# Kernel optimization log

Measured on AMD Instinct MI355X. Metric: run time of the kernel, lower is better.

## Reference

```python
import jax, jax.numpy as jnp
import numpy as np

NUM_HEADS = 16
BLOCK_KV = 64


def _split_heads(x, h):
    B, T, D = x.shape
    return x.reshape(B, T, h, D // h).transpose(0, 2, 1, 3)  # [B,H,T,Hd]


def _merge_heads(x):
    B, H, T, Hd = x.shape
    return x.transpose(0, 2, 1, 3).reshape(B, T, H * Hd)


def _streaming_attention(qh, kh, vh, bkv):
    # Online-softmax (flash-attention) over kv blocks; math identical to the
    # original nested-loop version (including the Z + 1e-9 denominator).
    B, H, T, Dh = qh.shape
    scale = 1.0 / jnp.sqrt(Dh).astype(jnp.float32)
    q32 = qh.astype(jnp.float32)
    nb = T // bkv
    # [nb, B, H, bkv, Dh]
    kb = jnp.moveaxis(kh.astype(jnp.float32).reshape(B, H, nb, bkv, Dh), 2, 0)
    vb = jnp.moveaxis(vh.astype(jnp.float32).reshape(B, H, nb, bkv, Dh), 2, 0)

    def step(carry, blk):
        m, Z, O = carry
        k_blk, v_blk = blk
        scores = jnp.einsum('bhtd,bhkd->bhtk', q32, k_blk) * scale
        m_new = jnp.maximum(m, jnp.max(scores, axis=-1, keepdims=True))
        alpha = jnp.exp(m - m_new)
        p = jnp.exp(scores - m_new)
        Z = Z * alpha + jnp.sum(p, axis=-1, keepdims=True)
        O = O * alpha + jnp.einsum('bhtk,bhkd->bhtd', p, v_blk)
        return (m_new, Z, O), None

    m0 = jnp.full((B, H, T, 1), -jnp.inf, dtype=jnp.float32)
    Z0 = jnp.zeros((B, H, T, 1), dtype=jnp.float32)
    O0 = jnp.zeros((B, H, T, Dh), dtype=jnp.float32)
    (m, Z, O), _ = jax.lax.scan(step, (m0, Z0, O0), (kb, vb))
    return (O / (Z + 1e-9)).astype(qh.dtype)


def setup_inputs() -> dict:
    key = jax.random.key(0)
    ks = jax.random.split(key, 6)
    B, T, D = 4, 8192, 512
    s = 1.0 / np.sqrt(D)
    return {
        'x': jax.random.normal(ks[0], (B, T, D), dtype=jnp.float32),
        'Wq': jax.random.normal(ks[1], (D, D), dtype=jnp.float32) * s,
        'Wk': jax.random.normal(ks[2], (D, D), dtype=jnp.float32) * s,
        'Wv': jax.random.normal(ks[3], (D, D), dtype=jnp.float32) * s,
        'Wo': jax.random.normal(ks[4], (D, D), dtype=jnp.float32) * s,
        'bo': jnp.zeros((D,), dtype=jnp.float32),
    }


def reference(x, Wq, Wk, Wv, Wo, bo):
    q = x @ Wq
    k = x @ Wk
    v = x @ Wv
    qh = _split_heads(q, NUM_HEADS)
    kh = _split_heads(k, NUM_HEADS)
    vh = _split_heads(v, NUM_HEADS)
    out_h = _streaming_attention(qh, kh, vh, BLOCK_KV)
    return _merge_heads(out_h) @ Wo + bo
```

## Files before the change

kernel.cpp:

```cpp
#include <hip/hip_runtime.h>
#include <hip/hip_bf16.h>
#include <math.h>

typedef __bf16 bf16;
typedef __bf16 bf16x2 __attribute__((ext_vector_type(2)));
typedef __bf16 bf16x4 __attribute__((ext_vector_type(4)));
typedef __bf16 bf16x8 __attribute__((ext_vector_type(8)));
typedef float f32x4 __attribute__((ext_vector_type(4)));
typedef unsigned int u32;
typedef u32 u32x4 __attribute__((ext_vector_type(4)));

#define B_ 4
#define T_ 8192
#define D_ 512
#define H_ 16
#define HD_ 32
#define M_ (B_ * T_)

#if __has_builtin(__builtin_amdgcn_exp2f)
#define EXP2(x) __builtin_amdgcn_exp2f(x)
#else
#define EXP2(x) exp2f(x)
#endif

#define LDSP(p) ((__attribute__((address_space(3))) void*)(p))
#define GLBP(p) ((const __attribute__((address_space(1))) void*)(p))

static __device__ __forceinline__ u32 pkbf16(float a, float b) {
  bf16x2 t;
  t[0] = (bf16)a;
  t[1] = (bf16)b;
  return __builtin_bit_cast(u32, t);
}

static __device__ __forceinline__ void swap32(u32& a, u32& b) {
#if __has_builtin(__builtin_amdgcn_permlane32_swap)
  auto r = __builtin_amdgcn_permlane32_swap(a, b, false, false);
  a = r[0];
  b = r[1];
#else
  asm volatile("v_permlane32_swap_b32 %0, %1" : "+v"(a), "+v"(b));
#endif
}

__global__ void k_cvt(const float* __restrict__ in, bf16* __restrict__ out, int n4) {
  int i = blockIdx.x * blockDim.x + threadIdx.x;
  const int stride = gridDim.x * blockDim.x;
  for (; i < n4; i += stride) {
    const float4 v = ((const float4*)in)[i];
    bf16x4 o;
    o.x = (bf16)v.x; o.y = (bf16)v.y; o.z = (bf16)v.z; o.w = (bf16)v.w;
    ((bf16x4*)out)[i] = o;
  }
}

__global__ void k_cvt_T(const float* __restrict__ w, bf16* __restrict__ wT, float scale) {
  const int tid = blockIdx.x * blockDim.x + threadIdx.x;
  const int n = tid >> 9, k = tid & 511;
  wT[tid] = (bf16)(w[k * 512 + n] * scale);
}

__global__ __launch_bounds__(256) void k_transposeV(const bf16* __restrict__ V,
                                                    bf16* __restrict__ VT) {
  __shared__ bf16 tile[128][36];
  const int bh = blockIdx.y, chunk = blockIdx.x;
  const int b = bh >> 4, h = bh & 15;
  const int kv0 = chunk * 128;
  const int tid = threadIdx.x;
  const int r = tid >> 1, c0 = (tid & 1) * 16;
  const size_t ib = ((size_t)(b * T_ + kv0 + r)) * 512 + h * 32 + c0;
  *(bf16x8*)&tile[r][c0]     = *(const bf16x8*)&V[ib];
  *(bf16x8*)&tile[r][c0 + 8] = *(const bf16x8*)&V[ib + 8];
  __syncthreads();
  const int d = tid >> 3, j0 = (tid & 7) * 16;
  bf16x8 o0, o1;
#pragma unroll
  for (int i = 0; i < 4; ++i) {
    o0[i]     = tile[j0 + i][d];
    o0[i + 4] = tile[j0 + 8 + i][d];
    o1[i]     = tile[j0 + 4 + i][d];
    o1[i + 4] = tile[j0 + 12 + i][d];
  }
  const size_t ob = ((size_t)bh * 32 + d) * T_ + kv0 + j0;
  *(bf16x8*)&VT[ob] = o0;
  *(bf16x8*)&VT[ob + 8] = o1;
}

template <int OUTF32>
__global__ __launch_bounds__(256) void k_gemm(const bf16* __restrict__ A,
                                              const bf16* __restrict__ BT,
                                              void* __restrict__ Cout,
                                              const float* __restrict__ bias) {
  __shared__ bf16 As[128][40];
  __shared__ bf16 Bs[128][40];
  const int bn = blockIdx.x * 128;
  const int bm = blockIdx.y * 128;
  const int tid = threadIdx.x;
  const int l = tid & 63, wid = tid >> 6;
  const int ln = l & 15, ku = l >> 4;
  const int wm = (wid >> 1) * 64, wn = (wid & 1) * 64;
  const int sr = tid >> 2, sc = (tid & 3) * 8;

  f32x4 acc[4][4] = {};

  for (int ks = 0; ks < 512; ks += 32) {
    __syncthreads();
    *(bf16x8*)&As[sr][sc]      = *(const bf16x8*)&A[(size_t)(bm + sr) * 512 + ks + sc];
    *(bf16x8*)&As[sr + 64][sc] = *(const bf16x8*)&A[(size_t)(bm + sr + 64) * 512 + ks + sc];
    *(bf16x8*)&Bs[sr][sc]      = *(const bf16x8*)&BT[(size_t)(bn + sr) * 512 + ks + sc];
    *(bf16x8*)&Bs[sr + 64][sc] = *(const bf16x8*)&BT[(size_t)(bn + sr + 64) * 512 + ks + sc];
    __syncthreads();

    bf16x8 af[4], bfr[4];
#pragma unroll
    for (int mt = 0; mt < 4; ++mt) af[mt] = *(const bf16x8*)&As[wm + mt * 16 + ln][ku * 8];
#pragma unroll
    for (int nt = 0; nt < 4; ++nt) bfr[nt] = *(const bf16x8*)&Bs[wn + nt * 16 + ln][ku * 8];
#pragma unroll
    for (int mt = 0; mt < 4; ++mt)
#pragma unroll
      for (int nt = 0; nt < 4; ++nt)
        acc[mt][nt] = __builtin_amdgcn_mfma_f32_16x16x32_bf16(af[mt], bfr[nt], acc[mt][nt], 0, 0, 0);
  }

#pragma unroll
  for (int mt = 0; mt < 4; ++mt)
#pragma unroll
    for (int nt = 0; nt < 4; ++nt)
#pragma unroll
      for (int r = 0; r < 4; ++r) {
        const int row = bm + wm + mt * 16 + ku * 4 + r;
        const int col = bn + wn + nt * 16 + ln;
        const float v = acc[mt][nt][r];
        if (OUTF32)
          ((float*)Cout)[(size_t)row * 512 + col] = v + bias[col];
        else
          ((bf16*)Cout)[(size_t)row * 512 + col] = (bf16)v;
      }
}

__global__ __launch_bounds__(256, 5) void k_attn(const bf16* __restrict__ Q,
                                                 const bf16* __restrict__ K,
                                                 const bf16* __restrict__ VT,
                                                 bf16* __restrict__ O) {
  __shared__ bf16 ks[2][2][64][32];
  __shared__ bf16 vts[2][2][32][64];
  const int qt = blockIdx.x;
  const int bh = blockIdx.y;
  const int b = bh >> 4, h = bh & 15;
  const size_t base = (size_t)b * T_ * 512 + (size_t)h * 32;
  const size_t vtbase = (size_t)bh * 32 * T_;
  const int tid = threadIdx.x;
  const int l = tid & 63, w = tid >> 6;
  const int ln = l & 15, ku = l >> 4;

  const int q0 = qt * 128 + w * 32;
  bf16x8 qf[2];
#pragma unroll
  for (int j = 0; j < 2; ++j)
    qf[j] = *(const bf16x8*)&Q[base + (size_t)(q0 + j * 16 + ln) * 512 + ku * 8];

  const u32 one2 = 0x3F803F80u;
  u32x4 onesu = {one2, one2, one2, one2};
  const bf16x8 ones = __builtin_bit_cast(bf16x8, onesu);

  const int krow = tid >> 2;
  const int kchS = ((tid & 3) ^ ((krow >> 1) & 3)) * 8;
  const int vrow = tid >> 3;
  const int vchS = ((tid & 7) ^ (vrow & 7)) * 8;
  const bf16* gk = K + base + (size_t)krow * 512 + kchS;
  const bf16* gv = VT + vtbase + (size_t)vrow * T_ + vchS;

  bf16* dk0 = &ks[0][0][w * 16][0];
  bf16* dk1 = &ks[1][0][w * 16][0];
  bf16* dv0 = &vts[0][0][w * 8][0];
  bf16* dv1 = &vts[1][0][w * 8][0];

  const char* ksr = (const char*)&ks[0][0][0][0] + ln * 64 + 16 * (ku ^ ((ln >> 1) & 3));
  const char* vr0 = (const char*)&vts[0][0][0][0] + ln * 128 + 16 * ((ku) ^ (ln & 7));
  const char* vr1 = (const char*)&vts[0][0][0][0] + ln * 128 + 16 * ((4 + ku) ^ (ln & 7));

  f32x4 o[2][2] = {};
  f32x4 zacc[2] = {};

  __builtin_amdgcn_global_load_lds(GLBP(gk), LDSP(dk0), 16, 0, 0);
  __builtin_amdgcn_global_load_lds(GLBP(gk + 32768), LDSP(dk0 + 2048), 16, 0, 0);
  __builtin_amdgcn_global_load_lds(GLBP(gv), LDSP(dv0), 16, 0, 0);
  __builtin_amdgcn_global_load_lds(GLBP(gv + 64), LDSP(dv0 + 2048), 16, 0, 0);
  gk += 2 * 64 * 512;
  gv += 128;
  __syncthreads();

#define KV_BODY2(CUR, DKN, DVN)                                                         \
  {                                                                                     \
    __builtin_amdgcn_global_load_lds(GLBP(gk), LDSP(DKN), 16, 0, 0);                    \
    __builtin_amdgcn_global_load_lds(GLBP(gk + 32768), LDSP(DKN + 2048), 16, 0, 0);     \
    __builtin_amdgcn_global_load_lds(GLBP(gv), LDSP(DVN), 16, 0, 0);                    \
    __builtin_amdgcn_global_load_lds(GLBP(gv + 64), LDSP(DVN + 2048), 16, 0, 0);        \
    gk += 2 * 64 * 512;                                                                 \
    gv += 128;                                                                          \
    _Pragma("unroll") for (int sub = 0; sub < 2; ++sub) {                               \
      _Pragma("unroll") for (int j = 0; j < 2; ++j) {                                   \
        _Pragma("unroll") for (int c = 0; c < 2; ++c) {                                 \
          const bf16x8 kf0 =                                                            \
              *(const bf16x8*)(ksr + (CUR)*8192 + sub * 4096 + c * 2048);               \
          const bf16x8 kf1 =                                                            \
              *(const bf16x8*)(ksr + (CUR)*8192 + sub * 4096 + c * 2048 + 1024);        \
          const f32x4 zz = {};                                                          \
          f32x4 s0 = __builtin_amdgcn_mfma_f32_16x16x32_bf16(kf0, qf[j], zz, 0, 0, 0);  \
          f32x4 s1 = __builtin_amdgcn_mfma_f32_16x16x32_bf16(kf1, qf[j], zz, 0, 0, 0);  \
          u32 lo0 = pkbf16(EXP2(s0[0]), EXP2(s0[1]));                                   \
          u32 hi0 = pkbf16(EXP2(s0[2]), EXP2(s0[3]));                                   \
          u32 lo1 = pkbf16(EXP2(s1[0]), EXP2(s1[1]));                                   \
          u32 hi1 = pkbf16(EXP2(s1[2]), EXP2(s1[3]));                                   \
          swap32(lo0, lo1);                                                             \
          swap32(hi0, hi1);                                                             \
          u32x4 pd = {lo0, hi0, lo1, hi1};                                              \
          const bf16x8 pf = __builtin_bit_cast(bf16x8, pd);                             \
          const bf16x8 va0 =                                                            \
              *(const bf16x8*)((c ? vr1 : vr0) + (CUR)*8192 + sub * 4096);              \
          const bf16x8 va1 =                                                            \
              *(const bf16x8*)((c ? vr1 : vr0) + (CUR)*8192 + sub * 4096 + 2048);       \
          o[j][0] = __builtin_amdgcn_mfma_f32_16x16x32_bf16(va0, pf, o[j][0], 0, 0, 0); \
          o[j][1] = __builtin_amdgcn_mfma_f32_16x16x32_bf16(va1, pf, o[j][1], 0, 0, 0); \
          zacc[j] =                                                                     \
              __builtin_amdgcn_mfma_f32_16x16x32_bf16(ones, pf, zacc[j], 0, 0, 0);      \
        }                                                                               \
      }                                                                                 \
    }                                                                                   \
    __syncthreads();                                                                    \
  }

  for (int kb = 0; kb < 128; kb += 4) {
    KV_BODY2(0, dk1, dv1);
    KV_BODY2(1, dk0, dv0);
  }
#undef KV_BODY2

#pragma unroll
  for (int j = 0; j < 2; ++j) {
    const float iz = 1.0f / (zacc[j][0] + 1e-9f);
    bf16x4 w0, w1;
#pragma unroll
    for (int r = 0; r < 4; ++r) {
      w0[r] = (bf16)(o[j][0][r] * iz);
      w1[r] = (bf16)(o[j][1][r] * iz);
    }
    const size_t row = base + (size_t)(q0 + j * 16 + ln) * 512;
    *(bf16x4*)&O[row + ku * 4] = w0;
    *(bf16x4*)&O[row + 16 + ku * 4] = w1;
  }
}

extern "C" void kernel_launch(void* const* d_in, const int* in_sizes, int n_in,
                              void* d_out, int out_size, void* d_ws, size_t ws_size,
                              hipStream_t stream) {
  const float* x = (const float*)d_in[0];
  const float* Wq = (const float*)d_in[1];
  const float* Wk = (const float*)d_in[2];
  const float* Wv = (const float*)d_in[3];
  const float* Wo = (const float*)d_in[4];
  const float* bo = (const float*)d_in[5];
  float* out = (float*)d_out;

  char* ws = (char*)d_ws;
  const size_t SZ = (size_t)M_ * 512 * sizeof(bf16);
  bf16* xb = (bf16*)(ws);
  bf16* qb = (bf16*)(ws + SZ);
  bf16* kb = (bf16*)(ws + 2 * SZ);
  bf16* vb = (bf16*)(ws + 3 * SZ);
  bf16* ob = (bf16*)(ws + 4 * SZ);
  bf16* wqT = (bf16*)(ws + 5 * SZ);
  bf16* wkT = wqT + 512 * 512;
  bf16* wvT = wkT + 512 * 512;
  bf16* woT = wvT + 512 * 512;
  bf16* vt = xb;

  const float SCALE_L2E = 0.17677669529663687f * 1.4426950408889634f;

  k_cvt<<<2048, 256, 0, stream>>>(x, xb, M_ * 512 / 4);
  k_cvt_T<<<1024, 256, 0, stream>>>(Wq, wqT, SCALE_L2E);
  k_cvt_T<<<1024, 256, 0, stream>>>(Wk, wkT, 1.0f);
  k_cvt_T<<<1024, 256, 0, stream>>>(Wv, wvT, 1.0f);
  k_cvt_T<<<1024, 256, 0, stream>>>(Wo, woT, 1.0f);

  dim3 gg(4, 256);
  k_gemm<0><<<gg, 256, 0, stream>>>(xb, wqT, qb, nullptr);
  k_gemm<0><<<gg, 256, 0, stream>>>(xb, wkT, kb, nullptr);
  k_gemm<0><<<gg, 256, 0, stream>>>(xb, wvT, vb, nullptr);

  dim3 gt(64, 64);
  k_transposeV<<<gt, 256, 0, stream>>>(vb, vt);
  dim3 ga(64, 64);
  k_attn<<<ga, 256, 0, stream>>>(qb, kb, vt, ob);

  k_gemm<1><<<gg, 256, 0, stream>>>(ob, woT, out, bo);
}
```

Baseline: 821.5 us.

## Fuse Q/K/V projections into one GEMM and prioritize MFMA waves in attention

```diff
diff --git a/kernel.cpp b/kernel.cpp
--- a/kernel.cpp
+++ b/kernel.cpp
@@ -16,6 +16,7 @@
 #define H_ 16
 #define HD_ 32
 #define M_ (B_ * T_)
+#define QKVS 1536
 
 #if __has_builtin(__builtin_amdgcn_exp2f)
 #define EXP2(x) __builtin_amdgcn_exp2f(x)
@@ -54,13 +55,23 @@
   }
 }
 
+__global__ void k_cvt_T3(const float* __restrict__ Wq, const float* __restrict__ Wk,
+                         const float* __restrict__ Wv, bf16* __restrict__ wT,
+                         float scaleq) {
+  const int tid = blockIdx.x * blockDim.x + threadIdx.x;
+  const int n = tid >> 9, k = tid & 511;
+  const float* W = (n < 512) ? Wq : ((n < 1024) ? Wk : Wv);
+  const float sc = (n < 512) ? scaleq : 1.0f;
+  wT[tid] = (bf16)(W[k * 512 + (n & 511)] * sc);
+}
+
 __global__ void k_cvt_T(const float* __restrict__ w, bf16* __restrict__ wT, float scale) {
   const int tid = blockIdx.x * blockDim.x + threadIdx.x;
   const int n = tid >> 9, k = tid & 511;
   wT[tid] = (bf16)(w[k * 512 + n] * scale);
 }
 
-__global__ __launch_bounds__(256) void k_transposeV(const bf16* __restrict__ V,
+__global__ __launch_bounds__(256) void k_transposeV(const bf16* __restrict__ QKV,
                                                     bf16* __restrict__ VT) {
   __shared__ bf16 tile[128][36];
   const int bh = blockIdx.y, chunk = blockIdx.x;
@@ -68,9 +79,9 @@
   const int kv0 = chunk * 128;
   const int tid = threadIdx.x;
   const int r = tid >> 1, c0 = (tid & 1) * 16;
-  const size_t ib = ((size_t)(b * T_ + kv0 + r)) * 512 + h * 32 + c0;
-  *(bf16x8*)&tile[r][c0]     = *(const bf16x8*)&V[ib];
-  *(bf16x8*)&tile[r][c0 + 8] = *(const bf16x8*)&V[ib + 8];
+  const size_t ib = (size_t)(b * T_ + kv0 + r) * QKVS + 1024 + h * 32 + c0;
+  *(bf16x8*)&tile[r][c0]     = *(const bf16x8*)&QKV[ib];
+  *(bf16x8*)&tile[r][c0 + 8] = *(const bf16x8*)&QKV[ib + 8];
   __syncthreads();
   const int d = tid >> 3, j0 = (tid & 7) * 16;
   bf16x8 o0, o1;
@@ -90,7 +101,8 @@
 __global__ __launch_bounds__(256) void k_gemm(const bf16* __restrict__ A,
                                               const bf16* __restrict__ BT,
                                               void* __restrict__ Cout,
-                                              const float* __restrict__ bias) {
+                                              const float* __restrict__ bias,
+                                              int cstride) {
   __shared__ bf16 As[128][40];
   __shared__ bf16 Bs[128][40];
   const int bn = blockIdx.x * 128;
@@ -133,14 +145,13 @@
         const int col = bn + wn + nt * 16 + ln;
         const float v = acc[mt][nt][r];
         if (OUTF32)
-          ((float*)Cout)[(size_t)row * 512 + col] = v + bias[col];
+          ((float*)Cout)[(size_t)row * cstride + col] = v + bias[col];
         else
-          ((bf16*)Cout)[(size_t)row * 512 + col] = (bf16)v;
+          ((bf16*)Cout)[(size_t)row * cstride + col] = (bf16)v;
       }
 }
 
-__global__ __launch_bounds__(256, 5) void k_attn(const bf16* __restrict__ Q,
-                                                 const bf16* __restrict__ K,
+__global__ __launch_bounds__(256, 5) void k_attn(const bf16* __restrict__ QKV,
                                                  const bf16* __restrict__ VT,
                                                  bf16* __restrict__ O) {
   __shared__ bf16 ks[2][2][64][32];
@@ -148,7 +159,8 @@
   const int qt = blockIdx.x;
   const int bh = blockIdx.y;
   const int b = bh >> 4, h = bh & 15;
-  const size_t base = (size_t)b * T_ * 512 + (size_t)h * 32;
+  const size_t baseq = (size_t)b * T_ * QKVS + h * 32;
+  const size_t baseo = (size_t)b * T_ * 512 + h * 32;
   const size_t vtbase = (size_t)bh * 32 * T_;
   const int tid = threadIdx.x;
   const int l = tid & 63, w = tid >> 6;
@@ -158,7 +170,7 @@
   bf16x8 qf[2];
 #pragma unroll
   for (int j = 0; j < 2; ++j)
-    qf[j] = *(const bf16x8*)&Q[base + (size_t)(q0 + j * 16 + ln) * 512 + ku * 8];
+    qf[j] = *(const bf16x8*)&QKV[baseq + (size_t)(q0 + j * 16 + ln) * QKVS + ku * 8];
 
   const u32 one2 = 0x3F803F80u;
   u32x4 onesu = {one2, one2, one2, one2};
@@ -168,8 +180,9 @@
   const int kchS = ((tid & 3) ^ ((krow >> 1) & 3)) * 8;
   const int vrow = tid >> 3;
   const int vchS = ((tid & 7) ^ (vrow & 7)) * 8;
-  const bf16* gk = K + base + (size_t)krow * 512 + kchS;
+  const bf16* gk = QKV + baseq + 512 + (size_t)krow * QKVS + kchS;
   const bf16* gv = VT + vtbase + (size_t)vrow * T_ + vchS;
+  const int KSUB = 64 * QKVS;
 
   bf16* dk0 = &ks[0][0][w * 16][0];
   bf16* dk1 = &ks[1][0][w * 16][0];
@@ -184,20 +197,20 @@
   f32x4 zacc[2] = {};
 
   __builtin_amdgcn_global_load_lds(GLBP(gk), LDSP(dk0), 16, 0, 0);
-  __builtin_amdgcn_global_load_lds(GLBP(gk + 32768), LDSP(dk0 + 2048), 16, 0, 0);
+  __builtin_amdgcn_global_load_lds(GLBP(gk + KSUB), LDSP(dk0 + 2048), 16, 0, 0);
   __builtin_amdgcn_global_load_lds(GLBP(gv), LDSP(dv0), 16, 0, 0);
   __builtin_amdgcn_global_load_lds(GLBP(gv + 64), LDSP(dv0 + 2048), 16, 0, 0);
-  gk += 2 * 64 * 512;
+  gk += 2 * KSUB;
   gv += 128;
   __syncthreads();
 
 #define KV_BODY2(CUR, DKN, DVN)                                                         \
   {                                                                                     \
     __builtin_amdgcn_global_load_lds(GLBP(gk), LDSP(DKN), 16, 0, 0);                    \
-    __builtin_amdgcn_global_load_lds(GLBP(gk + 32768), LDSP(DKN + 2048), 16, 0, 0);     \
+    __builtin_amdgcn_global_load_lds(GLBP(gk + KSUB), LDSP(DKN + 2048), 16, 0, 0);      \
     __builtin_amdgcn_global_load_lds(GLBP(gv), LDSP(DVN), 16, 0, 0);                    \
     __builtin_amdgcn_global_load_lds(GLBP(gv + 64), LDSP(DVN + 2048), 16, 0, 0);        \
-    gk += 2 * 64 * 512;                                                                 \
+    gk += 2 * KSUB;                                                                     \
     gv += 128;                                                                          \
     _Pragma("unroll") for (int sub = 0; sub < 2; ++sub) {                               \
       _Pragma("unroll") for (int j = 0; j < 2; ++j) {                                   \
@@ -207,8 +220,10 @@
           const bf16x8 kf1 =                                                            \
               *(const bf16x8*)(ksr + (CUR)*8192 + sub * 4096 + c * 2048 + 1024);        \
           const f32x4 zz = {};                                                          \
+          __builtin_amdgcn_s_setprio(1);                                                \
           f32x4 s0 = __builtin_amdgcn_mfma_f32_16x16x32_bf16(kf0, qf[j], zz, 0, 0, 0);  \
           f32x4 s1 = __builtin_amdgcn_mfma_f32_16x16x32_bf16(kf1, qf[j], zz, 0, 0, 0);  \
+          __builtin_amdgcn_s_setprio(0);                                                \
           u32 lo0 = pkbf16(EXP2(s0[0]), EXP2(s0[1]));                                   \
           u32 hi0 = pkbf16(EXP2(s0[2]), EXP2(s0[3]));                                   \
           u32 lo1 = pkbf16(EXP2(s1[0]), EXP2(s1[1]));                                   \
@@ -221,10 +236,12 @@
               *(const bf16x8*)((c ? vr1 : vr0) + (CUR)*8192 + sub * 4096);              \
           const bf16x8 va1 =                                                            \
               *(const bf16x8*)((c ? vr1 : vr0) + (CUR)*8192 + sub * 4096 + 2048);       \
+          __builtin_amdgcn_s_setprio(1);                                                \
           o[j][0] = __builtin_amdgcn_mfma_f32_16x16x32_bf16(va0, pf, o[j][0], 0, 0, 0); \
           o[j][1] = __builtin_amdgcn_mfma_f32_16x16x32_bf16(va1, pf, o[j][1], 0, 0, 0); \
           zacc[j] =                                                                     \
               __builtin_amdgcn_mfma_f32_16x16x32_bf16(ones, pf, zacc[j], 0, 0, 0);      \
+          __builtin_amdgcn_s_setprio(0);                                                \
         }                                                                               \
       }                                                                                 \
     }                                                                                   \
@@ -246,7 +263,7 @@
       w0[r] = (bf16)(o[j][0][r] * iz);
       w1[r] = (bf16)(o[j][1][r] * iz);
     }
-    const size_t row = base + (size_t)(q0 + j * 16 + ln) * 512;
+    const size_t row = baseo + (size_t)(q0 + j * 16 + ln) * 512;
     *(bf16x4*)&O[row + ku * 4] = w0;
     *(bf16x4*)&O[row + 16 + ku * 4] = w1;
   }
@@ -266,33 +283,26 @@
   char* ws = (char*)d_ws;
   const size_t SZ = (size_t)M_ * 512 * sizeof(bf16);
   bf16* xb = (bf16*)(ws);
-  bf16* qb = (bf16*)(ws + SZ);
-  bf16* kb = (bf16*)(ws + 2 * SZ);
-  bf16* vb = (bf16*)(ws + 3 * SZ);
+  bf16* qkv = (bf16*)(ws + SZ);
   bf16* ob = (bf16*)(ws + 4 * SZ);
-  bf16* wqT = (bf16*)(ws + 5 * SZ);
-  bf16* wkT = wqT + 512 * 512;
-  bf16* wvT = wkT + 512 * 512;
-  bf16* woT = wvT + 512 * 512;
+  bf16* wqkvT = (bf16*)(ws + 5 * SZ);
+  bf16* woT = wqkvT + 1536 * 512;
   bf16* vt = xb;
 
   const float SCALE_L2E = 0.17677669529663687f * 1.4426950408889634f;
 
   k_cvt<<<2048, 256, 0, stream>>>(x, xb, M_ * 512 / 4);
-  k_cvt_T<<<1024, 256, 0, stream>>>(Wq, wqT, SCALE_L2E);
-  k_cvt_T<<<1024, 256, 0, stream>>>(Wk, wkT, 1.0f);
-  k_cvt_T<<<1024, 256, 0, stream>>>(Wv, wvT, 1.0f);
+  k_cvt_T3<<<3072, 256, 0, stream>>>(Wq, Wk, Wv, wqkvT, SCALE_L2E);
   k_cvt_T<<<1024, 256, 0, stream>>>(Wo, woT, 1.0f);
 
+  dim3 gq(12, 256);
+  k_gemm<0><<<gq, 256, 0, stream>>>(xb, wqkvT, qkv, nullptr, QKVS);
+
+  dim3 gt(64, 64);
+  k_transposeV<<<gt, 256, 0, stream>>>(qkv, vt);
+  dim3 ga(64, 64);
+  k_attn<<<ga, 256, 0, stream>>>(qkv, vt, ob);
+
   dim3 gg(4, 256);
-  k_gemm<0><<<gg, 256, 0, stream>>>(xb, wqT, qb, nullptr);
-  k_gemm<0><<<gg, 256, 0, stream>>>(xb, wkT, kb, nullptr);
-  k_gemm<0><<<gg, 256, 0, stream>>>(xb, wvT, vb, nullptr);
-
-  dim3 gt(64, 64);
-  k_transposeV<<<gt, 256, 0, stream>>>(vb, vt);
-  dim3 ga(64, 64);
-  k_attn<<<ga, 256, 0, stream>>>(qb, kb, vt, ob);
-
-  k_gemm<1><<<gg, 256, 0, stream>>>(ob, woT, out, bo);
-}
+  k_gemm<1><<<gg, 256, 0, stream>>>(ob, woT, out, bo, 512);
+}
```

Result: no change. 832.8 us (+1.4%).
